# Kernel optimization log

Hardware: AMD Instinct MI355X
Metric: run time of the kernel (lower is better)

The kernel has to match this reference:

```python
import jax, jax.numpy as jnp
import numpy as np

HEADS = 16
DIM_HEAD = 64
SCALE = DIM_HEAD ** -0.5


def setup_inputs() -> dict:
    key = jax.random.key(0)
    k1, k2, k3 = jax.random.split(key, 3)
    dim, inner = 1024, HEADS * DIM_HEAD
    b, n = 2, 2048
    x = jax.random.normal(k1, (b, n, dim), dtype=jnp.float32)
    w_qkv = jax.random.normal(k2, (dim, 3 * inner), dtype=jnp.float32) * (dim ** -0.5)
    w_out = jax.random.normal(k3, (inner, dim), dtype=jnp.float32) * (inner ** -0.5)
    b_out = jnp.zeros((dim,), dtype=jnp.float32)
    return {"x": x, "w_qkv": w_qkv, "w_out": w_out, "b_out": b_out}


def reference(x, w_qkv, w_out, b_out):
    b, n, _ = x.shape
    qkv = x @ w_qkv                                   # [b,n,3*inner]
    q, k, v = jnp.split(qkv, 3, axis=-1)
    def to_heads(t):
        return t.reshape(b, n, HEADS, DIM_HEAD).transpose(0, 2, 1, 3)  # [b,h,n,d]
    q, k, v = to_heads(q), to_heads(k), to_heads(v)
    dots = jnp.einsum('bhid,bhjd->bhij', q, k) * SCALE  # [b,h,n,n]
    attn = jax.nn.softmax(dots, axis=-1)
    out = jnp.einsum('bhij,bhjd->bhid', attn, v)        # [b,h,n,d]
    out = out.transpose(0, 2, 1, 3).reshape(b, n, HEADS * DIM_HEAD)
    return out @ w_out + b_out
```

## Files before the change

kernel.cpp:

```cpp
#include <hip/hip_runtime.h>
#include <hip/hip_bf16.h>

typedef unsigned short u16;
typedef unsigned int u32;
typedef __attribute__((ext_vector_type(8))) short short8;
typedef __attribute__((ext_vector_type(4))) float f32x4;
typedef __attribute__((ext_vector_type(16))) float f32x16;
typedef __attribute__((ext_vector_type(2))) u32 u32x2;

__device__ __forceinline__ u16 f2b(float x) {
    union { float f; u32 u; } c; c.f = x;
    u32 r = c.u + 0x7fffu + ((c.u >> 16) & 1u);
    return (u16)(r >> 16);
}
__device__ __forceinline__ float b2f(u16 x) {
    union { u32 u; float f; } c; c.u = ((u32)x) << 16;
    return c.f;
}
__device__ __forceinline__ u32 cvtpk(float lo, float hi) {
    u32 r;
    asm("v_cvt_pk_bf16_f32 %0, %1, %2" : "=v"(r) : "v"(lo), "v"(hi));
    return r;
}

__global__ __launch_bounds__(256) void convert_cvt(const float* __restrict__ in,
                                                   u16* __restrict__ out, int n8) {
    int i = blockIdx.x * 256 + threadIdx.x;
    if (i >= n8) return;
    const float4* p = (const float4*)(in + (size_t)i * 8);
    float4 a = p[0], b = p[1];
    short8 v;
    v[0]=(short)f2b(a.x); v[1]=(short)f2b(a.y); v[2]=(short)f2b(a.z); v[3]=(short)f2b(a.w);
    v[4]=(short)f2b(b.x); v[5]=(short)f2b(b.y); v[6]=(short)f2b(b.z); v[7]=(short)f2b(b.w);
    *(short8*)(out + (size_t)i * 8) = v;
}

__global__ __launch_bounds__(256) void transpose_cvt(const float* __restrict__ in,
                                                     u16* __restrict__ out, int R, int C) {
    __shared__ u16 tile[64][72];
    const int t = threadIdx.x;
    const int r0 = blockIdx.y * 64, c0 = blockIdx.x * 64;
    {
        const int rr = t >> 2;
        const int cq = (t & 3) * 16;
        const float* src = in + (size_t)(r0 + rr) * C + c0 + cq;
        #pragma unroll
        for (int j = 0; j < 4; j++) {
            float4 v = *(const float4*)(src + j * 4);
            tile[cq + j*4 + 0][rr] = f2b(v.x);
            tile[cq + j*4 + 1][rr] = f2b(v.y);
            tile[cq + j*4 + 2][rr] = f2b(v.z);
            tile[cq + j*4 + 3][rr] = f2b(v.w);
        }
    }
    __syncthreads();
    {
        const int cc = t >> 2;
        const int rq = (t & 3) * 16;
        u16* dst = out + (size_t)(c0 + cc) * R + r0 + rq;
        *(short8*)(dst)     = *(const short8*)&tile[cc][rq];
        *(short8*)(dst + 8) = *(const short8*)&tile[cc][rq + 8];
    }
}

__global__ __launch_bounds__(256) void transpose_v_kernel(const u16* __restrict__ qkv,
                                                          u16* __restrict__ vt) {
    __shared__ u16 tile[64][72];
    const int t = threadIdx.x;
    const int n0 = blockIdx.x * 64;
    const int h = blockIdx.y, b = blockIdx.z;
    {
        const int nn = t >> 2;
        const int dq = (t & 3) * 16;
        const u16* src = qkv + (size_t)(b * 2048 + n0 + nn) * 3072 + 2048 + h * 64 + dq;
        #pragma unroll
        for (int j = 0; j < 2; j++) {
            short8 v = *(const short8*)(src + j * 8);
            #pragma unroll
            for (int e = 0; e < 8; e++) tile[dq + j*8 + e][nn] = (u16)v[e];
        }
    }
    __syncthreads();
    {
        const int dd = t >> 2;
        const int nq = (t & 3) * 16;
        u16* dst = vt + (size_t)((b * 16 + h) * 64 + dd) * 2048 + n0 + nq;
        *(short8*)(dst)     = *(const short8*)&tile[dd][nq];
        *(short8*)(dst + 8) = *(const short8*)&tile[dd][nq + 8];
    }
}

template<bool OUT_BF16>
__global__ __launch_bounds__(256) void gemm128(const u16* __restrict__ A,
                                               const u16* __restrict__ Bt,
                                               void* __restrict__ Cp,
                                               const float* __restrict__ bias,
                                               int M, int Nn, int K) {
    __shared__ u16 a_lds[128][40];
    __shared__ u16 b_lds[128][40];
    const int tid = threadIdx.x;
    const int w = tid >> 6, l = tid & 63;
    const int l16 = l & 15, lg = l >> 4;
    const int m0 = blockIdx.y * 128, n0 = blockIdx.x * 128;
    const int wm = w >> 1, wn = w & 1;
    const int srow = tid >> 2;
    const int skc  = (tid & 3) * 8;

    f32x4 acc[4][4];
    #pragma unroll
    for (int i = 0; i < 4; i++)
        #pragma unroll
        for (int j = 0; j < 4; j++) { f32x4 z = {0.f,0.f,0.f,0.f}; acc[i][j] = z; }

    const u16* Ap = A  + (size_t)m0 * K;
    const u16* Bp = Bt + (size_t)n0 * K;

    short8 ra[2], rb[2];
    #pragma unroll
    for (int i = 0; i < 2; i++) {
        ra[i] = *(const short8*)(Ap + (size_t)(i * 64 + srow) * K + skc);
        rb[i] = *(const short8*)(Bp + (size_t)(i * 64 + srow) * K + skc);
    }

    const int nk = K >> 5;
    for (int kt = 0; kt < nk; kt++) {
        __syncthreads();
        #pragma unroll
        for (int i = 0; i < 2; i++) {
            *(short8*)&a_lds[i * 64 + srow][skc] = ra[i];
            *(short8*)&b_lds[i * 64 + srow][skc] = rb[i];
        }
        __syncthreads();
        if (kt + 1 < nk) {
            const int k0 = (kt + 1) << 5;
            #pragma unroll
            for (int i = 0; i < 2; i++) {
                ra[i] = *(const short8*)(Ap + (size_t)(i * 64 + srow) * K + k0 + skc);
                rb[i] = *(const short8*)(Bp + (size_t)(i * 64 + srow) * K + k0 + skc);
            }
        }
        short8 af[4], bf8[4];
        #pragma unroll
        for (int mb = 0; mb < 4; mb++)
            af[mb] = *(const short8*)&a_lds[wm * 64 + mb * 16 + l16][lg * 8];
        #pragma unroll
        for (int nb = 0; nb < 4; nb++)
            bf8[nb] = *(const short8*)&b_lds[wn * 64 + nb * 16 + l16][lg * 8];
        #pragma unroll
        for (int mb = 0; mb < 4; mb++)
            #pragma unroll
            for (int nb = 0; nb < 4; nb++)
                acc[mb][nb] = __builtin_amdgcn_mfma_f32_16x16x32_bf16(af[mb], bf8[nb], acc[mb][nb], 0, 0, 0);
    }

    #pragma unroll
    for (int mb = 0; mb < 4; mb++) {
        #pragma unroll
        for (int nb = 0; nb < 4; nb++) {
            const int col = n0 + wn * 64 + nb * 16 + l16;
            #pragma unroll
            for (int r = 0; r < 4; r++) {
                const int row = m0 + wm * 64 + mb * 16 + lg * 4 + r;
                if constexpr (OUT_BF16) {
                    ((u16*)Cp)[(size_t)row * Nn + col] = f2b(acc[mb][nb][r]);
                } else {
                    ((float*)Cp)[(size_t)row * Nn + col] = acc[mb][nb][r] + bias[col];
                }
            }
        }
    }
}

__global__ __launch_bounds__(512, 2) void attn_kernel(const u16* __restrict__ qkv,
                                                      const u16* __restrict__ vt,
                                                      u16* __restrict__ out) {
    __shared__ __align__(16) u16 k_lds[8192];
    __shared__ __align__(16) u16 v_lds[8192];
    const int tid = threadIdx.x;
    const int w = tid >> 6, l = tid & 63;
    const int l31 = l & 31, hi = l >> 5;
    const int bb = blockIdx.z, h = blockIdx.y;
    const int q0 = blockIdx.x * 256 + w * 32;
    const int swzl = (l31 & 7) << 3;

    const u16* qp = qkv + (size_t)(bb * 2048 + q0 + l31) * 3072 + h * 64 + hi * 8;
    short8 qf[4];
    #pragma unroll
    for (int c4 = 0; c4 < 4; c4++) {
        short8 v = *(const short8*)(qp + c4 * 16);
        #pragma unroll
        for (int e = 0; e < 8; e++) v[e] = (short)f2b(b2f((u16)v[e]) * 0.125f);
        qf[c4] = v;
    }

    f32x16 o[2];
    #pragma unroll
    for (int d0 = 0; d0 < 2; d0++)
        #pragma unroll
        for (int e = 0; e < 16; e++) o[d0][e] = 0.f;
    float mrow = -1e30f, lsum = 0.f;

    const int srow = tid >> 3, scol = tid & 7;
    const int kd = srow * 64 + ((scol ^ (srow & 7)) * 8);
    const u16* ksrc = qkv + (size_t)(bb * 2048 + srow) * 3072 + 1024 + h * 64 + scol * 8;
    const u16* vsrc = vt + (size_t)((bb * 16 + h) * 64 + srow) * 2048 + scol * 8;

    short8 krg = *(const short8*)ksrc;
    short8 vrg = *(const short8*)vsrc;
    ksrc += 64 * 3072; vsrc += 64;
    *(short8*)&k_lds[kd] = krg;
    *(short8*)&v_lds[kd] = vrg;
    __syncthreads();

#define DO_TILE(CUR, NXT)                                                               \
  {                                                                                     \
     \
    krg = *(const short8*)ksrc; vrg = *(const short8*)vsrc;                             \
    ksrc += 64 * 3072; vsrc += 64;                                                      \
    f32x16 st[2];                                                                       \
    _Pragma("unroll") for (int tt = 0; tt < 2; tt++)                                    \
      _Pragma("unroll") for (int e = 0; e < 16; e++) st[tt][e] = 0.f;                   \
    _Pragma("unroll")                                                                   \
    for (int c4 = 0; c4 < 4; c4++) {                                                    \
      short8 kf0 = *(const short8*)&k_lds[(CUR) + (l31)*64      + ((c4*16 + hi*8) ^ swzl)]; \
      short8 kf1 = *(const short8*)&k_lds[(CUR) + (32 + l31)*64 + ((c4*16 + hi*8) ^ swzl)]; \
      st[0] = __builtin_amdgcn_mfma_f32_32x32x16_bf16(kf0, qf[c4], st[0], 0, 0, 0);     \
      st[1] = __builtin_amdgcn_mfma_f32_32x32x16_bf16(kf1, qf[c4], st[1], 0, 0, 0);     \
    }                                                                                   \
    float pmax = st[0][0];                                                              \
    _Pragma("unroll") for (int e = 1; e < 16; e++) pmax = fmaxf(pmax, st[0][e]);        \
    _Pragma("unroll") for (int e = 0; e < 16; e++) pmax = fmaxf(pmax, st[1][e]);        \
    const float rowm = fmaxf(pmax, __shfl_xor(pmax, 32));                               \
    if (__any(rowm > mrow + 5.5451774f)) {              \
      const float mnew  = fmaxf(mrow, rowm);                                            \
      const float alpha = __expf(mrow - mnew);                                          \
      lsum *= alpha;                                                                    \
      _Pragma("unroll") for (int d0 = 0; d0 < 2; d0++)                                  \
        _Pragma("unroll") for (int e = 0; e < 16; e++) o[d0][e] *= alpha;               \
      mrow = mnew;                                                                      \
    }                                                                                   \
    _Pragma("unroll") for (int tt = 0; tt < 2; tt++)                                    \
      _Pragma("unroll") for (int e = 0; e < 16; e++) st[tt][e] = __expf(st[tt][e] - mrow); \
    float psum = 0.f;                                                                   \
    _Pragma("unroll") for (int tt = 0; tt < 2; tt++)                                    \
      _Pragma("unroll") for (int e = 0; e < 16; e++) psum += st[tt][e];                 \
    lsum += psum + __shfl_xor(psum, 32);                                                \
    short8 pb[4];                                                                       \
    _Pragma("unroll")                                                                   \
    for (int tt = 0; tt < 2; tt++) {                                                    \
      _Pragma("unroll")                                                                 \
      for (int g = 0; g < 2; g++) {                                                     \
         \
        u32 w0 = cvtpk(st[tt][8*g + 0], st[tt][8*g + 1]);                               \
        u32 w1 = cvtpk(st[tt][8*g + 2], st[tt][8*g + 3]);                               \
        u32 w2 = cvtpk(st[tt][8*g + 4], st[tt][8*g + 5]);                               \
        u32 w3 = cvtpk(st[tt][8*g + 6], st[tt][8*g + 7]);                               \
        u32 w0x = (u32)__shfl_xor((int)w0, 32);                                         \
        u32 w1x = (u32)__shfl_xor((int)w1, 32);                                         \
        u32 w2x = (u32)__shfl_xor((int)w2, 32);                                         \
        u32 w3x = (u32)__shfl_xor((int)w3, 32);                                         \
        union { u32 wd[4]; short8 s8; } uu;                                             \
        uu.wd[0] = hi ? w2x : w0;                                                       \
        uu.wd[1] = hi ? w3x : w1;                                                       \
        uu.wd[2] = hi ? w2  : w0x;                                                      \
        uu.wd[3] = hi ? w3  : w1x;                                                      \
        pb[2*tt + g] = uu.s8;                                                           \
      }                                                                                 \
    }                                                                                   \
    _Pragma("unroll")                                                                   \
    for (int ks = 0; ks < 4; ks++) {                                                    \
      short8 vf0 = *(const short8*)&v_lds[(CUR) + (l31)*64      + ((ks*16 + hi*8) ^ swzl)]; \
      short8 vf1 = *(const short8*)&v_lds[(CUR) + (32 + l31)*64 + ((ks*16 + hi*8) ^ swzl)]; \
      o[0] = __builtin_amdgcn_mfma_f32_32x32x16_bf16(vf0, pb[ks], o[0], 0, 0, 0);       \
      o[1] = __builtin_amdgcn_mfma_f32_32x32x16_bf16(vf1, pb[ks], o[1], 0, 0, 0);       \
    }                                                                                   \
    *(short8*)&k_lds[(NXT) + kd] = krg;                                                 \
    *(short8*)&v_lds[(NXT) + kd] = vrg;                                                 \
    __syncthreads();                                                                    \
  }

    for (int it = 0; it < 16; it++) {
        DO_TILE(0, 4096)
        DO_TILE(4096, 0)
    }
#undef DO_TILE

    const float invl = 1.0f / lsum;
    u16* op = out + (size_t)(bb * 2048 + q0 + l31) * 1024 + h * 64;
    #pragma unroll
    for (int d0 = 0; d0 < 2; d0++) {
        #pragma unroll
        for (int s = 0; s < 4; s++) {
            u32x2 pr;
            pr.x = cvtpk(o[d0][4*s + 0] * invl, o[d0][4*s + 1] * invl);
            pr.y = cvtpk(o[d0][4*s + 2] * invl, o[d0][4*s + 3] * invl);
            *(u32x2*)(op + d0 * 32 + s * 8 + hi * 4) = pr;
        }
    }
}

extern "C" void kernel_launch(void* const* d_in, const int* in_sizes, int n_in,
                              void* d_out, int out_size, void* d_ws, size_t ws_size,
                              hipStream_t stream) {
    const float* x     = (const float*)d_in[0];
    const float* w_qkv = (const float*)d_in[1];
    const float* w_out = (const float*)d_in[2];
    const float* b_out = (const float*)d_in[3];

    char* ws = (char*)d_ws;
    u16* xb    = (u16*)(ws);
    u16* wqkvT = (u16*)(ws + (size_t)( 8u << 20));
    u16* woutT = (u16*)(ws + (size_t)(14u << 20));
    u16* qkvb  = (u16*)(ws + (size_t)(16u << 20));
    u16* vtb   = (u16*)(ws + (size_t)(40u << 20));
    u16* aout  = (u16*)(ws + (size_t)(48u << 20));

    convert_cvt<<<2048, 256, 0, stream>>>(x, xb, 4096 * 1024 / 8);
    transpose_cvt<<<dim3(48, 16), 256, 0, stream>>>(w_qkv, wqkvT, 1024, 3072);
    transpose_cvt<<<dim3(16, 16), 256, 0, stream>>>(w_out, woutT, 1024, 1024);

    gemm128<true><<<dim3(24, 32), 256, 0, stream>>>(xb, wqkvT, qkvb, nullptr,
                                                    4096, 3072, 1024);
    transpose_v_kernel<<<dim3(32, 16, 2), 256, 0, stream>>>(qkvb, vtb);
    attn_kernel<<<dim3(8, 16, 2), 512, 0, stream>>>(qkvb, vtb, aout);

    gemm128<false><<<dim3(8, 32), 256, 0, stream>>>(aout, woutT, d_out, b_out,
                                                    4096, 1024, 1024);
}
```

Before: 131.4 us.

## Fuse V transpose into QKV GEMM epilogue and use direct global-to-LDS loads

The QKV GEMM epilogue now writes the V columns straight into the transposed per-head layout, so the separate transpose_v kernel and its extra read/write pass go away. The GEMM mainloop also changes from register-staged prefetch to global_load_lds, which writes directly into unpadded LDS tiles, with a vmcnt wait before each barrier. This removes the register round-trip, but it also drops the software prefetch overlap: each K step now waits for its own loads. The unpadded LDS layout may add bank conflicts on fragment reads.

```diff
diff --git a/kernel.cpp b/kernel.cpp
--- a/kernel.cpp
+++ b/kernel.cpp
@@ -8,6 +8,9 @@
 typedef __attribute__((ext_vector_type(16))) float f32x16;
 typedef __attribute__((ext_vector_type(2))) u32 u32x2;
 
+typedef __attribute__((address_space(1))) void as1_void;
+typedef __attribute__((address_space(3))) void as3_void;
+
 __device__ __forceinline__ u16 f2b(float x) {
     union { float f; u32 u; } c; c.f = x;
     u32 r = c.u + 0x7fffu + ((c.u >> 16) & 1u);
@@ -21,6 +24,9 @@
     u32 r;
     asm("v_cvt_pk_bf16_f32 %0, %1, %2" : "=v"(r) : "v"(lo), "v"(hi));
     return r;
+}
+__device__ __forceinline__ void gload16(const u16* g, u16* l) {
+    __builtin_amdgcn_global_load_lds((as1_void*)(u16*)g, (as3_void*)l, 16, 0, 0);
 }
 
 __global__ __launch_bounds__(256) void convert_cvt(const float* __restrict__ in,
@@ -63,48 +69,22 @@
     }
 }
 
-__global__ __launch_bounds__(256) void transpose_v_kernel(const u16* __restrict__ qkv,
-                                                          u16* __restrict__ vt) {
-    __shared__ u16 tile[64][72];
-    const int t = threadIdx.x;
-    const int n0 = blockIdx.x * 64;
-    const int h = blockIdx.y, b = blockIdx.z;
-    {
-        const int nn = t >> 2;
-        const int dq = (t & 3) * 16;
-        const u16* src = qkv + (size_t)(b * 2048 + n0 + nn) * 3072 + 2048 + h * 64 + dq;
-        #pragma unroll
-        for (int j = 0; j < 2; j++) {
-            short8 v = *(const short8*)(src + j * 8);
-            #pragma unroll
-            for (int e = 0; e < 8; e++) tile[dq + j*8 + e][nn] = (u16)v[e];
-        }
-    }
-    __syncthreads();
-    {
-        const int dd = t >> 2;
-        const int nq = (t & 3) * 16;
-        u16* dst = vt + (size_t)((b * 16 + h) * 64 + dd) * 2048 + n0 + nq;
-        *(short8*)(dst)     = *(const short8*)&tile[dd][nq];
-        *(short8*)(dst + 8) = *(const short8*)&tile[dd][nq + 8];
-    }
-}
-
-template<bool OUT_BF16>
+template<bool QKV_MODE>
 __global__ __launch_bounds__(256) void gemm128(const u16* __restrict__ A,
                                                const u16* __restrict__ Bt,
                                                void* __restrict__ Cp,
+                                               u16* __restrict__ vt,
                                                const float* __restrict__ bias,
                                                int M, int Nn, int K) {
-    __shared__ u16 a_lds[128][40];
-    __shared__ u16 b_lds[128][40];
+    __shared__ __align__(16) u16 a_lds[128 * 32];
+    __shared__ __align__(16) u16 b_lds[128 * 32];
     const int tid = threadIdx.x;
     const int w = tid >> 6, l = tid & 63;
     const int l16 = l & 15, lg = l >> 4;
     const int m0 = blockIdx.y * 128, n0 = blockIdx.x * 128;
     const int wm = w >> 1, wn = w & 1;
-    const int srow = tid >> 2;
-    const int skc  = (tid & 3) * 8;
+    const int lr = l >> 2;
+    const int scol = (l & 3) * 8;
 
     f32x4 acc[4][4];
     #pragma unroll
@@ -115,37 +95,25 @@
     const u16* Ap = A  + (size_t)m0 * K;
     const u16* Bp = Bt + (size_t)n0 * K;
 
-    short8 ra[2], rb[2];
-    #pragma unroll
-    for (int i = 0; i < 2; i++) {
-        ra[i] = *(const short8*)(Ap + (size_t)(i * 64 + srow) * K + skc);
-        rb[i] = *(const short8*)(Bp + (size_t)(i * 64 + srow) * K + skc);
-    }
-
     const int nk = K >> 5;
     for (int kt = 0; kt < nk; kt++) {
+        const int kof = kt * 32;
         __syncthreads();
         #pragma unroll
-        for (int i = 0; i < 2; i++) {
-            *(short8*)&a_lds[i * 64 + srow][skc] = ra[i];
-            *(short8*)&b_lds[i * 64 + srow][skc] = rb[i];
+        for (int j = 0; j < 2; j++) {
+            const int r = w * 32 + j * 16;
+            gload16(Ap + (size_t)(r + lr) * K + kof + scol, &a_lds[r * 32]);
+            gload16(Bp + (size_t)(r + lr) * K + kof + scol, &b_lds[r * 32]);
         }
+        asm volatile("s_waitcnt vmcnt(0)" ::: "memory");
         __syncthreads();
-        if (kt + 1 < nk) {
-            const int k0 = (kt + 1) << 5;
-            #pragma unroll
-            for (int i = 0; i < 2; i++) {
-                ra[i] = *(const short8*)(Ap + (size_t)(i * 64 + srow) * K + k0 + skc);
-                rb[i] = *(const short8*)(Bp + (size_t)(i * 64 + srow) * K + k0 + skc);
-            }
-        }
         short8 af[4], bf8[4];
         #pragma unroll
         for (int mb = 0; mb < 4; mb++)
-            af[mb] = *(const short8*)&a_lds[wm * 64 + mb * 16 + l16][lg * 8];
+            af[mb] = *(const short8*)&a_lds[(wm * 64 + mb * 16 + l16) * 32 + lg * 8];
         #pragma unroll
         for (int nb = 0; nb < 4; nb++)
-            bf8[nb] = *(const short8*)&b_lds[wn * 64 + nb * 16 + l16][lg * 8];
+            bf8[nb] = *(const short8*)&b_lds[(wn * 64 + nb * 16 + l16) * 32 + lg * 8];
         #pragma unroll
         for (int mb = 0; mb < 4; mb++)
             #pragma unroll
@@ -158,14 +126,25 @@
         #pragma unroll
         for (int nb = 0; nb < 4; nb++) {
             const int col = n0 + wn * 64 + nb * 16 + l16;
-            #pragma unroll
-            for (int r = 0; r < 4; r++) {
-                const int row = m0 + wm * 64 + mb * 16 + lg * 4 + r;
-                if constexpr (OUT_BF16) {
-                    ((u16*)Cp)[(size_t)row * Nn + col] = f2b(acc[mb][nb][r]);
+            const int row0 = m0 + wm * 64 + mb * 16 + lg * 4;
+            if constexpr (QKV_MODE) {
+                if (col < 2048) {
+                    #pragma unroll
+                    for (int r = 0; r < 4; r++)
+                        ((u16*)Cp)[(size_t)(row0 + r) * Nn + col] = f2b(acc[mb][nb][r]);
                 } else {
-                    ((float*)Cp)[(size_t)row * Nn + col] = acc[mb][nb][r] + bias[col];
+                    const int hd = col - 2048;
+                    const int hh = hd >> 6, d = hd & 63;
+                    const int bi = row0 >> 11, n = row0 & 2047;
+                    u32x2 pr;
+                    pr.x = cvtpk(acc[mb][nb][0], acc[mb][nb][1]);
+                    pr.y = cvtpk(acc[mb][nb][2], acc[mb][nb][3]);
+                    *(u32x2*)(vt + ((size_t)((bi * 16 + hh) * 64 + d)) * 2048 + n) = pr;
                 }
+            } else {
+                #pragma unroll
+                for (int r = 0; r < 4; r++)
+                    ((float*)Cp)[(size_t)(row0 + r) * Nn + col] = acc[mb][nb][r] + bias[col];
             }
         }
     }
@@ -319,11 +298,10 @@
     transpose_cvt<<<dim3(48, 16), 256, 0, stream>>>(w_qkv, wqkvT, 1024, 3072);
     transpose_cvt<<<dim3(16, 16), 256, 0, stream>>>(w_out, woutT, 1024, 1024);
 
-    gemm128<true><<<dim3(24, 32), 256, 0, stream>>>(xb, wqkvT, qkvb, nullptr,
+    gemm128<true><<<dim3(24, 32), 256, 0, stream>>>(xb, wqkvT, qkvb, vtb, nullptr,
                                                     4096, 3072, 1024);
-    transpose_v_kernel<<<dim3(32, 16, 2), 256, 0, stream>>>(qkvb, vtb);
     attn_kernel<<<dim3(8, 16, 2), 512, 0, stream>>>(qkvb, vtb, aout);
 
-    gemm128<false><<<dim3(8, 32), 256, 0, stream>>>(aout, woutT, d_out, b_out,
+    gemm128<false><<<dim3(8, 32), 256, 0, stream>>>(aout, woutT, d_out, nullptr, b_out,
                                                     4096, 1024, 1024);
 }
```

Result: slower. 138.0 us (+5.0%).
